# Performance work log

Measured on AMD Instinct MI355X. Metric: run time of the kernel, lower is better.

## Reference

```python
import jax, jax.numpy as jnp
import numpy as np

B = 96   # batch (must equal C for the residual broadcast to be legal)
C = 96   # num_channels == seq_len (x is (B, C, 1, C))
S = 96   # sequence length = C
NH = 8   # num_heads
DK = 96  # d_k (defaults to num_channels)
G = 8    # groupnorm groups
EPS = 1e-5


def setup_inputs() -> dict:
    key = jax.random.key(0)
    ks = jax.random.split(key, 9)
    D = NH * DK
    scale = 0.05
    return {
        "x": jax.random.normal(ks[0], (B, C, 1, C), jnp.float32),
        "Wq": jax.random.normal(ks[1], (C, D), jnp.float32) * scale,
        "bq": jax.random.normal(ks[2], (D,), jnp.float32) * scale,
        "Wk": jax.random.normal(ks[3], (C, D), jnp.float32) * scale,
        "bk": jax.random.normal(ks[4], (D,), jnp.float32) * scale,
        "Wv": jax.random.normal(ks[5], (C, D), jnp.float32) * scale,
        "bv": jax.random.normal(ks[6], (D,), jnp.float32) * scale,
        "Wo": jax.random.normal(ks[7], (D, C), jnp.float32) * scale,
        "bo": jax.random.normal(ks[8], (C,), jnp.float32) * scale,
        "gamma": jnp.ones((C,), jnp.float32),
        "beta": jnp.zeros((C,), jnp.float32),
    }


def group_norm(x, gamma, beta):
    # x: (B, C, H, W); normalize over (C//G, H, W) within each of G groups
    b, c, h, w = x.shape
    xg = x.reshape(b, G, -1)
    mu = jnp.mean(xg, axis=-1, keepdims=True)
    var = jnp.var(xg, axis=-1, keepdims=True)
    xn = ((xg - mu) * jax.lax.rsqrt(var + EPS)).reshape(b, c, h, w)
    return xn * gamma[None, :, None, None] + beta[None, :, None, None]


def reference(x, Wq, bq, Wk, bk, Wv, bv, Wo, bo, gamma, beta):
    xn = group_norm(x, gamma, beta)           # (B, C, 1, C)
    residual = xn
    t = xn.reshape(B, S, C)                   # H == 1, squeeze
    # self-attention: q = k = v = normalized x
    q = (t @ Wq + bq).reshape(B, S, NH, DK).transpose(0, 2, 1, 3)  # (B, H, S, Dk)
    k = (t @ Wk + bk).reshape(B, S, NH, DK).transpose(0, 2, 1, 3)
    v = (t @ Wv + bv).reshape(B, S, NH, DK).transpose(0, 2, 1, 3)
    scores = jnp.einsum('bhqd,bhkd->bhqk', q, k) / jnp.sqrt(jnp.float32(DK))
    causal = jnp.tril(jnp.ones((S, S), bool))  # mask=True -> causal tril mask
    scores = jnp.where(causal[None, None], scores, -jnp.inf)
    attn = jax.nn.softmax(scores, axis=-1)
    out = jnp.einsum('bhqk,bhkd->bhqd', attn, v)       # (B, H, S, Dk)
    out = out.transpose(0, 2, 1, 3).reshape(B, S, NH * DK)
    out = out @ Wo + bo                                # (B, S, C); dropout(p=0) = id
    # faithful to the source: (B,S,C) + (B,C,1,C) broadcasts to (B,C,S,C)
    return out + residual
```

## Files before the change

### kernel.cpp

```cpp
#include <hip/hip_runtime.h>
#include <hip/hip_bf16.h>

#define BATCH 96
#define CH    96
#define SEQ   96
#define NHEAD 8
#define DK    96
#define DMODEL 768
#define GRP   8
#define EPSV  1e-5f

typedef __bf16 bf16x8 __attribute__((ext_vector_type(8)));
typedef float  f32x4  __attribute__((ext_vector_type(4)));
typedef unsigned short u16;

#define MFMA16(a, b, c) __builtin_amdgcn_mfma_f32_16x16x32_bf16((a), (b), (c), 0, 0, 0)

__device__ __forceinline__ u16 f2bf(float f) {
    union { float f; unsigned int u; } c; c.f = f;
    unsigned int u = c.u + 0x7fffu + ((c.u >> 16) & 1u);
    return (u16)(u >> 16);
}

__global__ __launch_bounds__(128) void gn_kernel(
        const float* __restrict__ x, const float* __restrict__ gamma,
        const float* __restrict__ beta, float* __restrict__ xn,
        u16* __restrict__ xn_bf) {
    int bg = blockIdx.x;
    int b = bg >> 3, g = bg & 7;
    const float* xp = x + b * 9216 + g * 1152;
    float vals[9];
    float s = 0.f, ss = 0.f;
    #pragma unroll
    for (int r = 0; r < 9; ++r) {
        float v = xp[threadIdx.x + 128 * r];
        vals[r] = v; s += v; ss += v * v;
    }
    #pragma unroll
    for (int off = 32; off > 0; off >>= 1) {
        s  += __shfl_down(s, off);
        ss += __shfl_down(ss, off);
    }
    __shared__ float red[4];
    if ((threadIdx.x & 63) == 0) {
        red[(threadIdx.x >> 6) * 2]     = s;
        red[(threadIdx.x >> 6) * 2 + 1] = ss;
    }
    __syncthreads();
    s = red[0] + red[2]; ss = red[1] + red[3];
    float mu   = s * (1.0f / 1152.0f);
    float var  = ss * (1.0f / 1152.0f) - mu * mu;
    float rsig = rsqrtf(var + EPSV);
    #pragma unroll
    for (int r = 0; r < 9; ++r) {
        int e = threadIdx.x + 128 * r;
        int c = g * 12 + e / 96;
        float v = (vals[r] - mu) * rsig * gamma[c] + beta[c];
        int idx = b * 9216 + g * 1152 + e;
        xn[idx]    = v;
        xn_bf[idx] = f2bf(v);
    }
}

__global__ __launch_bounds__(256) void wconv_kernel(
        const float* __restrict__ Wq, const float* __restrict__ Wk,
        const float* __restrict__ Wv, const float* __restrict__ Wo,
        u16* __restrict__ WqT, u16* __restrict__ WkT,
        u16* __restrict__ WvT, u16* __restrict__ WoT) {
    int seg = blockIdx.y;
    const float* src = seg == 0 ? Wq : seg == 1 ? Wk : seg == 2 ? Wv : Wo;
    u16* dst = seg == 0 ? WqT : seg == 1 ? WkT : seg == 2 ? WvT : WoT;
    int idx = blockIdx.x * 256 + threadIdx.x;
    if (idx < 73728) {
        if (seg < 3) {
            int n = idx / 96, k2 = idx - n * 96;
            dst[idx] = f2bf(src[k2 * 768 + n]);
        } else {
            int n = idx / 768, k2 = idx - n * 768;
            dst[idx] = f2bf(src[k2 * 96 + n]);
        }
    }
}

__global__ __launch_bounds__(384) void fattn_kernel(
        const u16* __restrict__ xn_bf,
        const u16* __restrict__ WqT, const u16* __restrict__ WkT,
        const u16* __restrict__ WvT,
        const float* __restrict__ bq, const float* __restrict__ bk,
        const float* __restrict__ bv,
        u16* __restrict__ attn_out) {
    int b = blockIdx.x >> 3, h = blockIdx.x & 7;
    __shared__ __align__(16) u16 qb[96][104];
    __shared__ __align__(16) u16 kb[96][104];
    __shared__ __align__(16) u16 vt[96][104];

    int wave = threadIdx.x >> 6, lane = threadIdx.x & 63;
    int ln = lane & 15, quad = lane >> 4;
    int m0 = wave * 16;
    const u16* xb = xn_bf + b * 9216;
    const int hq = h * 96;

    bf16x8 a[3], av[3];
    #pragma unroll
    for (int kt = 0; kt < 3; ++kt) {
        a[kt]  = *(const bf16x8*)(xb + (m0 + ln) * 96 + kt * 32 + quad * 8);
        av[kt] = *(const bf16x8*)(WvT + (hq + m0 + ln) * 96 + kt * 32 + quad * 8);
    }
    f32x4 aq[6] = {}, ak[6] = {}, avv[6] = {};
    #pragma unroll
    for (int kt = 0; kt < 3; ++kt) {
        #pragma unroll
        for (int nt = 0; nt < 6; ++nt) {
            bf16x8 bqf = *(const bf16x8*)(WqT + (hq + nt * 16 + ln) * 96 + kt * 32 + quad * 8);
            aq[nt] = MFMA16(a[kt], bqf, aq[nt]);
            bf16x8 bkf = *(const bf16x8*)(WkT + (hq + nt * 16 + ln) * 96 + kt * 32 + quad * 8);
            ak[nt] = MFMA16(a[kt], bkf, ak[nt]);
            bf16x8 bvf = *(const bf16x8*)(xb + (nt * 16 + ln) * 96 + kt * 32 + quad * 8);
            avv[nt] = MFMA16(av[kt], bvf, avv[nt]);
        }
    }
    float bvr[4];
    #pragma unroll
    for (int r = 0; r < 4; ++r) bvr[r] = bv[hq + m0 + quad * 4 + r];
    #pragma unroll
    for (int nt = 0; nt < 6; ++nt) {
        int col = nt * 16 + ln;
        float bqc = bq[hq + col], bkc = bk[hq + col];
        #pragma unroll
        for (int r = 0; r < 4; ++r) {
            int row = m0 + quad * 4 + r;
            qb[row][col] = f2bf(aq[nt][r] + bqc);
            kb[row][col] = f2bf(ak[nt][r] + bkc);
            vt[row][col] = f2bf(avv[nt][r] + bvr[r]);
        }
    }
    __syncthreads();

    f32x4 accs[6] = {};
    #pragma unroll
    for (int kt = 0; kt < 3; ++kt) {
        bf16x8 aa = *(const bf16x8*)(&qb[m0 + ln][kt * 32 + quad * 8]);
        #pragma unroll
        for (int nt = 0; nt < 6; ++nt) {
            bf16x8 bb = *(const bf16x8*)(&kb[nt * 16 + ln][kt * 32 + quad * 8]);
            accs[nt] = MFMA16(aa, bb, accs[nt]);
        }
    }

    const float scale = 0.10206207261596577f;
    float pout[4][6];
    #pragma unroll
    for (int r = 0; r < 4; ++r) {
        int row = m0 + quad * 4 + r;
        float vals[6], m = -1e30f;
        #pragma unroll
        for (int nt = 0; nt < 6; ++nt) {
            int col = nt * 16 + ln;
            float sv = accs[nt][r] * scale;
            vals[nt] = (col <= row) ? sv : -1e30f;
            m = fmaxf(m, vals[nt]);
        }
        #pragma unroll
        for (int off = 1; off < 16; off <<= 1) m = fmaxf(m, __shfl_xor(m, off));
        float sum = 0.f;
        #pragma unroll
        for (int nt = 0; nt < 6; ++nt) {
            float p = (vals[nt] > -1e29f) ? __expf(vals[nt] - m) : 0.f;
            pout[r][nt] = p; sum += p;
        }
        #pragma unroll
        for (int off = 1; off < 16; off <<= 1) sum += __shfl_xor(sum, off);
        float rinv = 1.0f / sum;
        #pragma unroll
        for (int nt = 0; nt < 6; ++nt) pout[r][nt] *= rinv;
    }
    __syncthreads();
    #pragma unroll
    for (int r = 0; r < 4; ++r)
        #pragma unroll
        for (int nt = 0; nt < 6; ++nt)
            kb[m0 + quad * 4 + r][nt * 16 + ln] = f2bf(pout[r][nt]);
    __syncthreads();

    f32x4 acco[6] = {};
    #pragma unroll
    for (int kt = 0; kt < 3; ++kt) {
        bf16x8 aa = *(const bf16x8*)(&kb[m0 + ln][kt * 32 + quad * 8]);
        #pragma unroll
        for (int nt = 0; nt < 6; ++nt) {
            bf16x8 bb = *(const bf16x8*)(&vt[nt * 16 + ln][kt * 32 + quad * 8]);
            acco[nt] = MFMA16(aa, bb, acco[nt]);
        }
    }
    const size_t obase = (size_t)b * 96 * DMODEL + hq;
    #pragma unroll
    for (int nt = 0; nt < 6; ++nt) {
        int d = nt * 16 + ln;
        #pragma unroll
        for (int r = 0; r < 4; ++r) {
            int row = m0 + quad * 4 + r;
            attn_out[obase + (size_t)row * DMODEL + d] = f2bf(acco[nt][r]);
        }
    }
}

__global__ __launch_bounds__(256) void oproj_kernel(
        const u16* __restrict__ attn, const u16* __restrict__ WoT,
        const float* __restrict__ bo, float* __restrict__ proj) {
    int wave = threadIdx.x >> 6, lane = threadIdx.x & 63;
    int ln = lane & 15, quad = lane >> 4;
    int m0 = blockIdx.x * 16;
    int k0 = wave * 192;
    f32x4 acc[6] = {};
    #pragma unroll
    for (int kt = 0; kt < 6; ++kt) {
        bf16x8 a = *(const bf16x8*)(attn + (size_t)(m0 + ln) * DMODEL + k0 + kt * 32 + quad * 8);
        #pragma unroll
        for (int nt = 0; nt < 6; ++nt) {
            bf16x8 bb = *(const bf16x8*)(WoT + (nt * 16 + ln) * DMODEL + k0 + kt * 32 + quad * 8);
            acc[nt] = MFMA16(a, bb, acc[nt]);
        }
    }
    __shared__ float red[4][16][96];
    #pragma unroll
    for (int nt = 0; nt < 6; ++nt)
        #pragma unroll
        for (int r = 0; r < 4; ++r)
            red[wave][quad * 4 + r][nt * 16 + ln] = acc[nt][r];
    __syncthreads();
    #pragma unroll
    for (int e = 0; e < 6; ++e) {
        int idx = threadIdx.x + e * 256;
        int row = idx / 96, col = idx - row * 96;
        float s = red[0][row][col] + red[1][row][col] +
                  red[2][row][col] + red[3][row][col] + bo[col];
        proj[(m0 + row) * 96 + col] = s;
    }
}

__global__ __launch_bounds__(256) void bcast_kernel(
        const float* __restrict__ proj, const float* __restrict__ xn,
        float* __restrict__ out) {
    int i = blockIdx.x / 96, j = blockIdx.x - i * 96;
    __shared__ float4 xrow[24];
    if (threadIdx.x < 24)
        xrow[threadIdx.x] = ((const float4*)(xn + (i * 96 + j) * 96))[threadIdx.x];
    __syncthreads();
    const float4* p4 = (const float4*)proj + j * 2304;
    float4* o4 = (float4*)out + (size_t)(i * 96 + j) * 2304;
    #pragma unroll
    for (int it = 0; it < 9; ++it) {
        int idx = threadIdx.x + it * 256;
        int kk = idx / 24;
        int l4 = idx - kk * 24;
        float4 pv = p4[idx];
        float4 xv = xrow[l4];
        float4 rr;
        rr.x = pv.x + xv.x; rr.y = pv.y + xv.y;
        rr.z = pv.z + xv.z; rr.w = pv.w + xv.w;
        o4[idx] = rr;
    }
}

extern "C" void kernel_launch(void* const* d_in, const int* in_sizes, int n_in,
                              void* d_out, int out_size, void* d_ws, size_t ws_size,
                              hipStream_t stream) {
    const float* x     = (const float*)d_in[0];
    const float* Wq    = (const float*)d_in[1];
    const float* bq    = (const float*)d_in[2];
    const float* Wk    = (const float*)d_in[3];
    const float* bk    = (const float*)d_in[4];
    const float* Wv    = (const float*)d_in[5];
    const float* bv    = (const float*)d_in[6];
    const float* Wo    = (const float*)d_in[7];
    const float* bo    = (const float*)d_in[8];
    const float* gamma = (const float*)d_in[9];
    const float* beta  = (const float*)d_in[10];
    float* out = (float*)d_out;

    char* ws = (char*)d_ws;
    float* xn_f = (float*)(ws + 0);
    u16*  xn_b  = (u16*)(ws + 3538944);
    u16*  WqT   = (u16*)(ws + 5308416);
    u16*  WkT   = (u16*)(ws + 5455872);
    u16*  WvT   = (u16*)(ws + 5603328);
    u16*  WoT   = (u16*)(ws + 5750784);
    u16*  ab    = (u16*)(ws + 5898240);
    float* proj = (float*)(ws + 20054016);

    gn_kernel<<<dim3(BATCH * GRP), dim3(128), 0, stream>>>(x, gamma, beta, xn_f, xn_b);
    wconv_kernel<<<dim3(288, 4), dim3(256), 0, stream>>>(Wq, Wk, Wv, Wo, WqT, WkT, WvT, WoT);
    fattn_kernel<<<dim3(BATCH * NHEAD), dim3(384), 0, stream>>>(
        xn_b, WqT, WkT, WvT, bq, bk, bv, ab);
    oproj_kernel<<<dim3(576), dim3(256), 0, stream>>>(ab, WoT, bo, proj);
    bcast_kernel<<<dim3(96 * 96), dim3(256), 0, stream>>>(proj, xn_f, out);
}
```

Measured before the change: 430.0 us.

## Fuse output projection with residual broadcast and merge prep kernels

Merges the groupnorm and weight-conversion kernels into one launch, and fuses the output projection with the broadcast residual add. Each projection block keeps its 16x96 projected tile and a transposed xn slice in LDS, then writes its share of the large output directly with nontemporal stores. This removes the proj round trip and two launches. In exchange each block writes a much larger share of the output, and only 576 blocks handle the bandwidth-bound broadcast, so store parallelism may drop.

```diff
diff --git a/kernel.cpp b/kernel.cpp
--- a/kernel.cpp
+++ b/kernel.cpp
@@ -22,56 +22,55 @@
     return (u16)(u >> 16);
 }
 
-__global__ __launch_bounds__(128) void gn_kernel(
+__global__ __launch_bounds__(128) void prep_kernel(
         const float* __restrict__ x, const float* __restrict__ gamma,
-        const float* __restrict__ beta, float* __restrict__ xn,
-        u16* __restrict__ xn_bf) {
-    int bg = blockIdx.x;
-    int b = bg >> 3, g = bg & 7;
-    const float* xp = x + b * 9216 + g * 1152;
-    float vals[9];
-    float s = 0.f, ss = 0.f;
-    #pragma unroll
-    for (int r = 0; r < 9; ++r) {
-        float v = xp[threadIdx.x + 128 * r];
-        vals[r] = v; s += v; ss += v * v;
-    }
-    #pragma unroll
-    for (int off = 32; off > 0; off >>= 1) {
-        s  += __shfl_down(s, off);
-        ss += __shfl_down(ss, off);
-    }
-    __shared__ float red[4];
-    if ((threadIdx.x & 63) == 0) {
-        red[(threadIdx.x >> 6) * 2]     = s;
-        red[(threadIdx.x >> 6) * 2 + 1] = ss;
-    }
-    __syncthreads();
-    s = red[0] + red[2]; ss = red[1] + red[3];
-    float mu   = s * (1.0f / 1152.0f);
-    float var  = ss * (1.0f / 1152.0f) - mu * mu;
-    float rsig = rsqrtf(var + EPSV);
-    #pragma unroll
-    for (int r = 0; r < 9; ++r) {
-        int e = threadIdx.x + 128 * r;
-        int c = g * 12 + e / 96;
-        float v = (vals[r] - mu) * rsig * gamma[c] + beta[c];
-        int idx = b * 9216 + g * 1152 + e;
-        xn[idx]    = v;
-        xn_bf[idx] = f2bf(v);
-    }
-}
-
-__global__ __launch_bounds__(256) void wconv_kernel(
+        const float* __restrict__ beta,
         const float* __restrict__ Wq, const float* __restrict__ Wk,
         const float* __restrict__ Wv, const float* __restrict__ Wo,
+        float* __restrict__ xn, u16* __restrict__ xn_bf,
         u16* __restrict__ WqT, u16* __restrict__ WkT,
         u16* __restrict__ WvT, u16* __restrict__ WoT) {
-    int seg = blockIdx.y;
-    const float* src = seg == 0 ? Wq : seg == 1 ? Wk : seg == 2 ? Wv : Wo;
-    u16* dst = seg == 0 ? WqT : seg == 1 ? WkT : seg == 2 ? WvT : WoT;
-    int idx = blockIdx.x * 256 + threadIdx.x;
-    if (idx < 73728) {
+    if (blockIdx.x < 768) {
+        int bg = blockIdx.x;
+        int b = bg >> 3, g = bg & 7;
+        const float* xp = x + b * 9216 + g * 1152;
+        float vals[9];
+        float s = 0.f, ss = 0.f;
+        #pragma unroll
+        for (int r = 0; r < 9; ++r) {
+            float v = xp[threadIdx.x + 128 * r];
+            vals[r] = v; s += v; ss += v * v;
+        }
+        #pragma unroll
+        for (int off = 32; off > 0; off >>= 1) {
+            s  += __shfl_down(s, off);
+            ss += __shfl_down(ss, off);
+        }
+        __shared__ float red[4];
+        if ((threadIdx.x & 63) == 0) {
+            red[(threadIdx.x >> 6) * 2]     = s;
+            red[(threadIdx.x >> 6) * 2 + 1] = ss;
+        }
+        __syncthreads();
+        s = red[0] + red[2]; ss = red[1] + red[3];
+        float mu   = s * (1.0f / 1152.0f);
+        float var  = ss * (1.0f / 1152.0f) - mu * mu;
+        float rsig = rsqrtf(var + EPSV);
+        #pragma unroll
+        for (int r = 0; r < 9; ++r) {
+            int e = threadIdx.x + 128 * r;
+            int c = g * 12 + e / 96;
+            float v = (vals[r] - mu) * rsig * gamma[c] + beta[c];
+            int idx = b * 9216 + g * 1152 + e;
+            xn[idx]    = v;
+            xn_bf[idx] = f2bf(v);
+        }
+    } else {
+        int t = blockIdx.x - 768;
+        int seg = t / 576;
+        int idx = (t - seg * 576) * 128 + threadIdx.x;
+        const float* src = seg == 0 ? Wq : seg == 1 ? Wk : seg == 2 ? Wv : Wo;
+        u16* dst = seg == 0 ? WqT : seg == 1 ? WkT : seg == 2 ? WvT : WoT;
         if (seg < 3) {
             int n = idx / 96, k2 = idx - n * 96;
             dst[idx] = f2bf(src[k2 * 768 + n]);
@@ -204,61 +203,70 @@
     }
 }
 
-__global__ __launch_bounds__(256) void oproj_kernel(
+__global__ __launch_bounds__(256) void obcast_kernel(
         const u16* __restrict__ attn, const u16* __restrict__ WoT,
-        const float* __restrict__ bo, float* __restrict__ proj) {
+        const float* __restrict__ bo, const float* __restrict__ xn,
+        float* __restrict__ out) {
+    __shared__ __align__(16) float red[4][16][96];
+    __shared__ __align__(16) float xnt[96][96];
     int wave = threadIdx.x >> 6, lane = threadIdx.x & 63;
     int ln = lane & 15, quad = lane >> 4;
     int m0 = blockIdx.x * 16;
-    int k0 = wave * 192;
+    int j  = blockIdx.x / 6;
+    int k0 = (blockIdx.x - j * 6) * 16;
+
+    {
+        const f32x4* xn4 = (const f32x4*)xn;
+        f32x4* xt4 = (f32x4*)xnt;
+        #pragma unroll
+        for (int it = 0; it < 9; ++it) {
+            int idx = threadIdx.x + it * 256;
+            int i = idx / 24, l4 = idx - i * 24;
+            xt4[idx] = xn4[(size_t)(i * 96 + j) * 24 + l4];
+        }
+    }
+
+    int kw = wave * 192;
     f32x4 acc[6] = {};
     #pragma unroll
     for (int kt = 0; kt < 6; ++kt) {
-        bf16x8 a = *(const bf16x8*)(attn + (size_t)(m0 + ln) * DMODEL + k0 + kt * 32 + quad * 8);
-        #pragma unroll
-        for (int nt = 0; nt < 6; ++nt) {
-            bf16x8 bb = *(const bf16x8*)(WoT + (nt * 16 + ln) * DMODEL + k0 + kt * 32 + quad * 8);
+        bf16x8 a = *(const bf16x8*)(attn + (size_t)(m0 + ln) * DMODEL + kw + kt * 32 + quad * 8);
+        #pragma unroll
+        for (int nt = 0; nt < 6; ++nt) {
+            bf16x8 bb = *(const bf16x8*)(WoT + (nt * 16 + ln) * DMODEL + kw + kt * 32 + quad * 8);
             acc[nt] = MFMA16(a, bb, acc[nt]);
         }
     }
-    __shared__ float red[4][16][96];
     #pragma unroll
     for (int nt = 0; nt < 6; ++nt)
         #pragma unroll
         for (int r = 0; r < 4; ++r)
             red[wave][quad * 4 + r][nt * 16 + ln] = acc[nt][r];
     __syncthreads();
+
     #pragma unroll
     for (int e = 0; e < 6; ++e) {
         int idx = threadIdx.x + e * 256;
         int row = idx / 96, col = idx - row * 96;
-        float s = red[0][row][col] + red[1][row][col] +
-                  red[2][row][col] + red[3][row][col] + bo[col];
-        proj[(m0 + row) * 96 + col] = s;
-    }
-}
-
-__global__ __launch_bounds__(256) void bcast_kernel(
-        const float* __restrict__ proj, const float* __restrict__ xn,
-        float* __restrict__ out) {
-    int i = blockIdx.x / 96, j = blockIdx.x - i * 96;
-    __shared__ float4 xrow[24];
-    if (threadIdx.x < 24)
-        xrow[threadIdx.x] = ((const float4*)(xn + (i * 96 + j) * 96))[threadIdx.x];
-    __syncthreads();
-    const float4* p4 = (const float4*)proj + j * 2304;
-    float4* o4 = (float4*)out + (size_t)(i * 96 + j) * 2304;
-    #pragma unroll
-    for (int it = 0; it < 9; ++it) {
+        red[0][row][col] = red[0][row][col] + red[1][row][col] +
+                           red[2][row][col] + red[3][row][col] + bo[col];
+    }
+    __syncthreads();
+
+    f32x4* out4 = (f32x4*)out;
+    const f32x4* pt4 = (const f32x4*)red;
+    const f32x4* xt4 = (const f32x4*)xnt;
+    #pragma unroll 4
+    for (int it = 0; it < 144; ++it) {
         int idx = threadIdx.x + it * 256;
-        int kk = idx / 24;
-        int l4 = idx - kk * 24;
-        float4 pv = p4[idx];
-        float4 xv = xrow[l4];
-        float4 rr;
-        rr.x = pv.x + xv.x; rr.y = pv.y + xv.y;
-        rr.z = pv.z + xv.z; rr.w = pv.w + xv.w;
-        o4[idx] = rr;
+        int i = idx / 384;
+        int rem = idx - i * 384;
+        int k = rem / 24, l4 = rem - k * 24;
+        f32x4 pv = pt4[k * 24 + l4];
+        f32x4 xv = xt4[i * 24 + l4];
+        f32x4 rr = pv + xv;
+        __builtin_nontemporal_store(rr,
+            &out4[((size_t)(i * 96 + j) * 96 + (k0 + k)) * 24 + l4]);
     }
 }
 
@@ -286,12 +294,10 @@
     u16*  WvT   = (u16*)(ws + 5603328);
     u16*  WoT   = (u16*)(ws + 5750784);
     u16*  ab    = (u16*)(ws + 5898240);
-    float* proj = (float*)(ws + 20054016);
-
-    gn_kernel<<<dim3(BATCH * GRP), dim3(128), 0, stream>>>(x, gamma, beta, xn_f, xn_b);
-    wconv_kernel<<<dim3(288, 4), dim3(256), 0, stream>>>(Wq, Wk, Wv, Wo, WqT, WkT, WvT, WoT);
+
+    prep_kernel<<<dim3(3072), dim3(128), 0, stream>>>(
+        x, gamma, beta, Wq, Wk, Wv, Wo, xn_f, xn_b, WqT, WkT, WvT, WoT);
     fattn_kernel<<<dim3(BATCH * NHEAD), dim3(384), 0, stream>>>(
         xn_b, WqT, WkT, WvT, bq, bk, bv, ab);
-    oproj_kernel<<<dim3(576), dim3(256), 0, stream>>>(ab, WoT, bo, proj);
-    bcast_kernel<<<dim3(96 * 96), dim3(256), 0, stream>>>(proj, xn_f, out);
-}
+    obcast_kernel<<<dim3(576), dim3(256), 0, stream>>>(ab, WoT, bo, xn_f, out);
+}
```

New measurement: 415.7 us. 3.3% less time.
